# Performance work log

Hardware: AMD Instinct MI355X
Metric: run time of the kernel (lower is better)

## Reference

```python
import jax, jax.numpy as jnp
import numpy as np

B, R, T, F_IN, L, D, H, OUT, ES = 8, 128, 64, 32, 64, 64, 128, 32, 2048
DT = 0.1  # dt_step from init


def _glorot(key, shape):
    scale = 1.0 / np.sqrt(shape[0])
    return (jax.random.normal(key, shape, jnp.float32) * scale).astype(jnp.float32)


def setup_inputs() -> dict:
    key = jax.random.key(0)
    ks = jax.random.split(key, 20)
    return {
        "node_feats": jax.random.normal(ks[0], (B, R, T, F_IN), jnp.float32),
        "eps": jax.random.normal(ks[1], (B, R, L + D), jnp.float32),
        "space_w": jax.random.uniform(ks[2], (B, ES), jnp.float32),
        "src": jax.random.randint(ks[3], (ES,), 0, R, jnp.int32),
        "dst": jax.random.randint(ks[4], (ES,), 0, R, jnp.int32),
        "W_e1": _glorot(ks[5], (F_IN + 1, H)),
        "b_e1": jnp.zeros((H,), jnp.float32),
        "W_e2": _glorot(ks[6], (H, H)),
        "b_e2": jnp.zeros((H,), jnp.float32),
        "W_mu": _glorot(ks[7], (H, L + D)),
        "W_sig": _glorot(ks[8], (H, L + D)),
        "W_msg": _glorot(ks[9], (L, L)),
        "W_self": _glorot(ks[10], (L, L)),
        "W_dyn": _glorot(ks[11], (D, L)),
        "b_ode": jnp.zeros((L,), jnp.float32),
        "W_d1": _glorot(ks[12], (L + D + 1 + R, H)),
        "b_d1": jnp.zeros((H,), jnp.float32),
        "W_d2": _glorot(ks[13], (H, OUT)),
        "b_d2": jnp.zeros((OUT,), jnp.float32),
    }


def reference(node_feats, eps, space_w, src, dst,
              W_e1, b_e1, W_e2, b_e2, W_mu, W_sig,
              W_msg, W_self, W_dyn, b_ode,
              W_d1, b_d1, W_d2, b_d2):
    dt = jnp.asarray(DT, node_feats.dtype)
    tgrid = jnp.arange(T, dtype=node_feats.dtype) / T  # normalized time, like t/t.max()
    t_feat = jnp.broadcast_to(tgrid[None, None, :, None], (B, R, T, 1))

    # ---- Encoder: node features + time -> per-node mu/sigma (NP-style) ----
    x = jnp.concatenate([node_feats, t_feat], axis=-1)          # [B,R,T,F+1]
    h = jax.nn.silu(x @ W_e1 + b_e1)
    h = jax.nn.silu(h @ W_e2 + b_e2)
    hp = h.mean(axis=2)                                          # pool over time -> [B,R,H]
    mu = hp @ W_mu                                               # [B,R,L+D]
    sigma = 0.1 + 0.9 * jax.nn.sigmoid(hp @ W_sig)
    v = mu + sigma * eps                                         # reparameterized latent
    Lz, Dz = v[..., :L], v[..., L:]                              # integrated state / h_dyn

    # ---- MPGCN ODE func: weighted edge gather/scatter + self + h_dyn ----
    dyn = Dz @ W_dyn                                             # constant conditioning [B,R,L]

    def f(xs):                                                   # xs: [B,R,L]
        m = space_w[..., None] * xs[:, src, :]                   # per-edge message [B,E,L]
        agg = jnp.zeros((B, R, L), xs.dtype).at[:, dst].add(m)   # sum aggregation
        return jnp.tanh(agg @ W_msg + xs @ W_self + dyn + b_ode)

    # ---- RK4 fixed-step integrator, save state at every time point ----
    def step(xs, _):
        k1 = f(xs)
        k2 = f(xs + 0.5 * dt * k1)
        k3 = f(xs + 0.5 * dt * k2)
        k4 = f(xs + dt * k3)
        xn = xs + (dt / 6.0) * (k1 + 2.0 * k2 + 2.0 * k3 + k4)
        return xn, xn

    _, traj = jax.lax.scan(step, Lz, None, length=T)             # [T,B,R,L]
    traj = jnp.moveaxis(traj, 0, 2)                              # [B,R,T,L]

    # ---- Decoder: [L(t), h_dyn, time, region one-hot] -> y ----
    rid = jnp.broadcast_to(jnp.eye(R, dtype=traj.dtype)[None, :, None, :], (B, R, T, R))
    d_rep = jnp.broadcast_to(Dz[:, :, None, :], (B, R, T, D))
    dec_in = jnp.concatenate([traj, d_rep, t_feat, rid], axis=-1)  # [B,R,T,257]
    hd = jax.nn.silu(dec_in @ W_d1 + b_d1)
    y = hd @ W_d2 + b_d2                                         # [B,R,T,OUT]
    return y
```

## Files before the change

### kernel.cpp

```cpp
#include <hip/hip_runtime.h>

#define B_ 8
#define R_ 128
#define T_ 64
#define FIN_ 32
#define L_ 64
#define D_ 64
#define H_ 128
#define OUT_ 32
#define ES_ 2048

typedef _Float16 f16;
typedef __attribute__((ext_vector_type(2))) _Float16 f16x2;
typedef __attribute__((ext_vector_type(4))) _Float16 f16x4;
typedef __attribute__((ext_vector_type(8))) _Float16 f16x8;
typedef __attribute__((ext_vector_type(16))) float f32x16;

__device__ __forceinline__ float silu_f(float x) { return x / (1.f + __expf(-x)); }
__device__ __forceinline__ float tanh_f(float x) {
    float e = __expf(2.f * x);
    return 1.f - 2.f / (e + 1.f);
}

__device__ __forceinline__ uint32_t swz256(uint32_t row, uint32_t s, uint32_t colByte) {
    uint32_t bo = row * 256u + s * 128u + colByte;
    return bo ^ ((row & 15u) << 4);
}
__device__ __forceinline__ uint32_t swzT(uint32_t c, uint32_t s, uint32_t rByte) {
    uint32_t bo = c * 512u + s * 256u + rByte;
    return bo ^ ((c & 31u) << 4);
}

#define XROW_OFF 0u
#define MT_OFF   32768u
#define WS_OFF   65536u
#define WM_OFF   81920u
#define ODE_LDS  98304u

__global__ __launch_bounds__(128) void prep_kernel(
    const int* __restrict__ src, const int* __restrict__ dst,
    const float* __restrict__ space_w,
    int* __restrict__ row_start, int* __restrict__ esrcp, float* __restrict__ wperm) {
    __shared__ int cnt[R_];
    __shared__ int rs[R_ + 1];
    __shared__ int permS[ES_];
    int r = threadIdx.x;
    int c = 0;
    for (int e = 0; e < ES_; ++e) c += (dst[e] == r) ? 1 : 0;
    cnt[r] = c;
    __syncthreads();
    if (r == 0) {
        int a = 0;
        for (int i = 0; i < R_; ++i) { rs[i] = a; a += cnt[i]; }
        rs[R_] = a;
    }
    __syncthreads();
    {
        int k = rs[r];
        for (int e = 0; e < ES_; ++e)
            if (dst[e] == r) permS[k++] = e;
    }
    __syncthreads();
    row_start[r] = rs[r];
    if (r == 0) row_start[R_] = rs[R_];
    for (int e = r; e < ES_; e += 128) esrcp[e] = src[permS[e]];
    for (int i = r; i < B_ * ES_; i += 128) {
        int b = i >> 11;
        int e = i & (ES_ - 1);
        wperm[i] = space_w[b * ES_ + permS[e]];
    }
}

__global__ __launch_bounds__(256) void encoder_kernel(
    const float* __restrict__ node_feats, const float* __restrict__ eps,
    const float* __restrict__ W_e1, const float* __restrict__ b_e1,
    const float* __restrict__ W_e2, const float* __restrict__ b_e2,
    const float* __restrict__ W_mu, const float* __restrict__ W_sig,
    const float* __restrict__ W_dyn,
    float* __restrict__ Lz, float* __restrict__ Dz, float* __restrict__ dynb) {
    int br = blockIdx.x;
    int tid = threadIdx.x;
    __shared__ __align__(16) float xS[T_ * 36];
    __shared__ __align__(16) float h1[T_ * H_];
    __shared__ float hps[2 * H_];
    __shared__ float hp[H_];
    __shared__ float muS[H_], sgS[H_], vS[H_];

    const float* nf = node_feats + (size_t)br * (T_ * FIN_);
    for (int i = tid; i < T_ * FIN_; i += 256) {
        int t = i >> 5, f = i & 31;
        xS[t * 36 + f] = nf[i];
    }
    if (tid < T_) xS[tid * 36 + 32] = (float)tid * (1.f / 64.f);

    int j = tid & 127;
    int th = tid >> 7;
    float we1r[33];
    #pragma unroll
    for (int k = 0; k < 33; ++k) we1r[k] = W_e1[k * H_ + j];
    __syncthreads();

    float be1 = b_e1[j];
    for (int tt = 0; tt < 32; ++tt) {
        int t = th * 32 + tt;
        float a = be1;
        const float4* xr = (const float4*)(&xS[t * 36]);
        #pragma unroll
        for (int w4 = 0; w4 < 8; ++w4) {
            float4 xv = xr[w4];
            a += xv.x * we1r[w4 * 4 + 0] + xv.y * we1r[w4 * 4 + 1] +
                 xv.z * we1r[w4 * 4 + 2] + xv.w * we1r[w4 * 4 + 3];
        }
        a += xS[t * 36 + 32] * we1r[32];
        h1[t * H_ + j] = silu_f(a);
    }
    __syncthreads();

    float acc[32];
    float be2 = b_e2[j];
    #pragma unroll
    for (int tt = 0; tt < 32; ++tt) acc[tt] = be2;
    for (int kc = 0; kc < 4; ++kc) {
        float wreg[32];
        #pragma unroll
        for (int i2 = 0; i2 < 32; ++i2) wreg[i2] = W_e2[(kc * 32 + i2) * H_ + j];
        #pragma unroll
        for (int tt = 0; tt < 32; ++tt) {
            int t = th * 32 + tt;
            const float4* hrow = (const float4*)(&h1[t * H_ + kc * 32]);
            float s = 0.f;
            #pragma unroll
            for (int w4 = 0; w4 < 8; ++w4) {
                float4 hv = hrow[w4];
                s += hv.x * wreg[w4 * 4 + 0] + hv.y * wreg[w4 * 4 + 1] +
                     hv.z * wreg[w4 * 4 + 2] + hv.w * wreg[w4 * 4 + 3];
            }
            acc[tt] += s;
        }
    }
    float msum = 0.f;
    #pragma unroll
    for (int tt = 0; tt < 32; ++tt) msum += silu_f(acc[tt]);
    hps[th * H_ + j] = msum;
    __syncthreads();
    if (tid < H_) hp[tid] = (hps[tid] + hps[H_ + tid]) * (1.f / 64.f);
    __syncthreads();

    {
        const float* Wm = (th == 0) ? W_mu : W_sig;
        float a = 0.f;
        #pragma unroll 4
        for (int k = 0; k < H_; ++k) a += hp[k] * Wm[k * H_ + j];
        if (th == 0) muS[j] = a; else sgS[j] = a;
    }
    __syncthreads();
    if (tid < H_) {
        float sig = 0.1f + 0.9f / (1.f + __expf(-sgS[tid]));
        float v = muS[tid] + sig * eps[(size_t)br * H_ + tid];
        vS[tid] = v;
        if (tid < L_) Lz[(size_t)br * L_ + tid] = v;
        else          Dz[(size_t)br * D_ + (tid - L_)] = v;
    }
    __syncthreads();
    if (tid < L_) {
        float a = 0.f;
        #pragma unroll 4
        for (int k = 0; k < D_; ++k) a += vS[L_ + k] * W_dyn[k * L_ + tid];
        dynb[(size_t)br * L_ + tid] = a;
    }
}

__global__ __launch_bounds__(512, 2) void ode_kernel(
    const float* __restrict__ Lz, const float* __restrict__ dynb,
    const float* __restrict__ W_msg, const float* __restrict__ W_self,
    const float* __restrict__ b_ode,
    const int* __restrict__ row_start, const int* __restrict__ esrcp,
    const float* __restrict__ wperm,
    float* __restrict__ traj) {
    const int b = blockIdx.x;
    const int tid = threadIdx.x;
    const int lane = tid & 63;
    const int w = tid >> 6;
    const int rb = w & 3;
    const int cb = w >> 2;
    const int l31 = lane & 31;
    const int h = lane >> 5;
    const int cc = cb * 32 + l31;

    extern __shared__ char sm[];
    float* Af = (float*)sm;

    for (int idx = tid; idx < 4096; idx += 512) {
        int j = idx & 63, k = idx >> 6;
        float vs = W_self[k * 64 + j];
        f16 sh = (f16)vs;
        *(f16*)(sm + WS_OFF + swz256(j, 0, k * 2)) = sh;
        *(f16*)(sm + WS_OFF + swz256(j, 1, k * 2)) = (f16)(vs - (float)sh);
        float vm = W_msg[k * 64 + j];
        f16 mh = (f16)vm;
        *(f16*)(sm + WM_OFF + swz256(j, 0, k * 2)) = mh;
        *(f16*)(sm + WM_OFF + swz256(j, 1, k * 2)) = (f16)(vm - (float)mh);
    }
    for (int i = tid; i < 128 * 128; i += 512) Af[i] = 0.f;
    __syncthreads();
    if (tid < 128) {
        int e0 = row_start[tid], e1 = row_start[tid + 1];
        for (int e = e0; e < e1; ++e)
            Af[tid * 128 + esrcp[e]] += wperm[b * ES_ + e];
    }
    __syncthreads();

    f16x8 aH[8], aL[8];
    {
        int row = rb * 32 + l31;
        #pragma unroll
        for (int m = 0; m < 8; ++m) {
            const float* p = Af + row * 128 + m * 16 + h * 8;
            f16x8 vh, vl;
            #pragma unroll
            for (int i = 0; i < 8; ++i) {
                float v = p[i];
                f16 hi = (f16)v;
                vh[i] = hi;
                vl[i] = (f16)(v - (float)hi);
            }
            aH[m] = vh;
            aL[m] = vl;
        }
    }

    float xb[16], ks[16], dnb[16];
    {
        float bo = b_ode[cc];
        #pragma unroll
        for (int i = 0; i < 16; ++i) {
            int r = rb * 32 + (i & 3) + 8 * (i >> 2) + 4 * h;
            size_t o = ((size_t)(b * R_ + r)) * L_ + cc;
            xb[i] = Lz[o];
            dnb[i] = dynb[o] + bo;
        }
    }
    __syncthreads();

    #pragma unroll
    for (int i = 0; i < 16; ++i) {
        int r = rb * 32 + (i & 3) + 8 * (i >> 2) + 4 * h;
        f16 hi = (f16)xb[i];
        *(f16*)(sm + XROW_OFF + swz256(r, 0, cc * 2)) = hi;
        *(f16*)(sm + XROW_OFF + swz256(r, 1, cc * 2)) = (f16)(xb[i] - (float)hi);
    }
    __syncthreads();

    const int rowx = rb * 32 + l31;

    for (int n = 0; n < T_; ++n) {
        #pragma unroll
        for (int i = 0; i < 16; ++i) ks[i] = 0.f;
        for (int s4 = 0; s4 < 4; ++s4) {
            const float wk = (s4 == 1 || s4 == 2) ? 2.f : 1.f;
            const float cn = (s4 < 2) ? 0.05f : 0.1f;

            f16x8 xh[4], xl[4];
            #pragma unroll
            for (int m = 0; m < 4; ++m) {
                uint32_t kB = (m * 16 + 8 * h) * 2;
                xh[m] = *(const f16x8*)(sm + XROW_OFF + swz256(rowx, 0, kB));
                xl[m] = *(const f16x8*)(sm + XROW_OFF + swz256(rowx, 1, kB));
            }
            f32x16 aS, aM = {};
            #pragma unroll
            for (int i = 0; i < 16; ++i) aS[i] = dnb[i];
            #pragma unroll
            for (int m = 0; m < 4; ++m) {
                uint32_t kB = (m * 16 + 8 * h) * 2;
                f16x8 wsH = *(const f16x8*)(sm + WS_OFF + swz256(cc, 0, kB));
                f16x8 wsL = *(const f16x8*)(sm + WS_OFF + swz256(cc, 1, kB));
                f16x8 wmH = *(const f16x8*)(sm + WM_OFF + swz256(cc, 0, kB));
                f16x8 wmL = *(const f16x8*)(sm + WM_OFF + swz256(cc, 1, kB));
                aS = __builtin_amdgcn_mfma_f32_32x32x16_f16(xh[m], wsH, aS, 0, 0, 0);
                aM = __builtin_amdgcn_mfma_f32_32x32x16_f16(xh[m], wmH, aM, 0, 0, 0);
                aS = __builtin_amdgcn_mfma_f32_32x32x16_f16(xl[m], wsH, aS, 0, 0, 0);
                aM = __builtin_amdgcn_mfma_f32_32x32x16_f16(xl[m], wmH, aM, 0, 0, 0);
                aS = __builtin_amdgcn_mfma_f32_32x32x16_f16(xh[m], wsL, aS, 0, 0, 0);
                aM = __builtin_amdgcn_mfma_f32_32x32x16_f16(xh[m], wmL, aM, 0, 0, 0);
            }
            #pragma unroll
            for (int q = 0; q < 4; ++q) {
                int rbase = rb * 32 + 8 * q + 4 * h;
                f16x4 vh, vl;
                #pragma unroll
                for (int u = 0; u < 4; ++u) {
                    float t = aM[4 * q + u];
                    f16 hi = (f16)t;
                    vh[u] = hi;
                    vl[u] = (f16)(t - (float)hi);
                }
                *(f16x4*)(sm + MT_OFF + swzT(cc, 0, rbase * 2)) = vh;
                *(f16x4*)(sm + MT_OFF + swzT(cc, 1, rbase * 2)) = vl;
            }
            __syncthreads();

            f32x16 e0 = {}, e1 = {}, e2 = {};
            #pragma unroll
            for (int m = 0; m < 8; ++m) {
                f16x8 mtH = *(const f16x8*)(sm + MT_OFF + swzT(cc, 0, (m * 16 + 8 * h) * 2));
                f16x8 mtL = *(const f16x8*)(sm + MT_OFF + swzT(cc, 1, (m * 16 + 8 * h) * 2));
                if (m < 3) {
                    e0 = __builtin_amdgcn_mfma_f32_32x32x16_f16(aH[m], mtH, e0, 0, 0, 0);
                    e0 = __builtin_amdgcn_mfma_f32_32x32x16_f16(aL[m], mtH, e0, 0, 0, 0);
                    e0 = __builtin_amdgcn_mfma_f32_32x32x16_f16(aH[m], mtL, e0, 0, 0, 0);
                } else if (m < 6) {
                    e1 = __builtin_amdgcn_mfma_f32_32x32x16_f16(aH[m], mtH, e1, 0, 0, 0);
                    e1 = __builtin_amdgcn_mfma_f32_32x32x16_f16(aL[m], mtH, e1, 0, 0, 0);
                    e1 = __builtin_amdgcn_mfma_f32_32x32x16_f16(aH[m], mtL, e1, 0, 0, 0);
                } else {
                    e2 = __builtin_amdgcn_mfma_f32_32x32x16_f16(aH[m], mtH, e2, 0, 0, 0);
                    e2 = __builtin_amdgcn_mfma_f32_32x32x16_f16(aL[m], mtH, e2, 0, 0, 0);
                    e2 = __builtin_amdgcn_mfma_f32_32x32x16_f16(aH[m], mtL, e2, 0, 0, 0);
                }
            }
            float xn_[16];
            #pragma unroll
            for (int i = 0; i < 16; ++i) {
                float kv = tanh_f(aS[i] + e0[i] + e1[i] + e2[i]);
                ks[i] += wk * kv;
                xn_[i] = (s4 < 3) ? (xb[i] + cn * kv) : (xb[i] + (0.1f / 6.f) * ks[i]);
            }
            if (s4 == 3) {
                #pragma unroll
                for (int i = 0; i < 16; ++i) xb[i] = xn_[i];
            }
            #pragma unroll
            for (int i = 0; i < 16; ++i) {
                int r = rb * 32 + (i & 3) + 8 * (i >> 2) + 4 * h;
                f16 hi = (f16)xn_[i];
                *(f16*)(sm + XROW_OFF + swz256(r, 0, cc * 2)) = hi;
                *(f16*)(sm + XROW_OFF + swz256(r, 1, cc * 2)) = (f16)(xn_[i] - (float)hi);
            }
            if (s4 == 3) {
                #pragma unroll
                for (int i = 0; i < 16; ++i) {
                    int r = rb * 32 + (i & 3) + 8 * (i >> 2) + 4 * h;
                    traj[(((size_t)b * T_ + n) * R_ + r) * L_ + cc] = xb[i];
                }
            }
            __syncthreads();
        }
    }
}

__global__ __launch_bounds__(256) void decoder_kernel(
    const float* __restrict__ traj, const float* __restrict__ Dz,
    const float* __restrict__ W_d1, const float* __restrict__ b_d1,
    const float* __restrict__ W_d2, const float* __restrict__ b_d2,
    float* __restrict__ y) {
    int br = blockIdx.x;
    int b = br >> 7;
    int r = br & 127;
    int tid = threadIdx.x;
    __shared__ __align__(16) float trajS[32 * L_];
    __shared__ __align__(16) float hS[32 * H_];
    __shared__ float dzS[D_];
    __shared__ float baseS[H_];

    int j = tid & 127;
    int th = tid >> 7;
    if (tid < D_) dzS[tid] = Dz[(size_t)br * D_ + tid];
    __syncthreads();

    float wcol[64];
    #pragma unroll
    for (int k = 0; k < 64; ++k) wcol[k] = W_d1[k * H_ + j];
    float wt = W_d1[128 * H_ + j];
    if (th == 0) {
        float a = b_d1[j] + W_d1[(129 + r) * H_ + j];
        #pragma unroll 4
        for (int k = 0; k < D_; ++k) a += dzS[k] * W_d1[(64 + k) * H_ + j];
        baseS[j] = a;
    }
    __syncthreads();
    float bb = baseS[j];

    for (int half = 0; half < 2; ++half) {
        for (int i = tid; i < 32 * L_; i += 256) {
            int tt = i >> 6, l = i & 63;
            trajS[i] = traj[(((size_t)b * T_ + half * 32 + tt) * R_ + r) * L_ + l];
        }
        __syncthreads();
        #pragma unroll
        for (int tt = 0; tt < 16; ++tt) {
            int tl = th * 16 + tt;
            int t = half * 32 + tl;
            float a = bb + (float)t * (1.f / 64.f) * wt;
            const float4* tr4 = (const float4*)(&trajS[tl * L_]);
            #pragma unroll
            for (int kb = 0; kb < 16; ++kb) {
                float4 tv = tr4[kb];
                a += tv.x * wcol[kb * 4 + 0] + tv.y * wcol[kb * 4 + 1] +
                     tv.z * wcol[kb * 4 + 2] + tv.w * wcol[kb * 4 + 3];
            }
            hS[tl * H_ + j] = silu_f(a);
        }
        __syncthreads();
        {
            int o = tid & 31, q = tid >> 5;
            float acc2[4];
            float bd2 = b_d2[o];
            #pragma unroll
            for (int u = 0; u < 4; ++u) acc2[u] = bd2;
            for (int jc = 0; jc < 4; ++jc) {
                float wreg[32];
                #pragma unroll
                for (int i2 = 0; i2 < 32; ++i2) wreg[i2] = W_d2[(jc * 32 + i2) * OUT_ + o];
                #pragma unroll
                for (int u = 0; u < 4; ++u) {
                    int tl = q * 4 + u;
                    const float4* h4 = (const float4*)(&hS[tl * H_ + jc * 32]);
                    float s2 = 0.f;
                    #pragma unroll
                    for (int w4 = 0; w4 < 8; ++w4) {
                        float4 hv = h4[w4];
                        s2 += hv.x * wreg[w4 * 4 + 0] + hv.y * wreg[w4 * 4 + 1] +
                              hv.z * wreg[w4 * 4 + 2] + hv.w * wreg[w4 * 4 + 3];
                    }
                    acc2[u] += s2;
                }
            }
            #pragma unroll
            for (int u = 0; u < 4; ++u) {
                int t = half * 32 + q * 4 + u;
                y[((size_t)br * T_ + t) * OUT_ + o] = acc2[u];
            }
        }
        __syncthreads();
    }
}

extern "C" void kernel_launch(void* const* d_in, const int* in_sizes, int n_in,
                              void* d_out, int out_size, void* d_ws, size_t ws_size,
                              hipStream_t stream) {
    const float* node_feats = (const float*)d_in[0];
    const float* eps_       = (const float*)d_in[1];
    const float* space_w    = (const float*)d_in[2];
    const int*   src        = (const int*)d_in[3];
    const int*   dst        = (const int*)d_in[4];
    const float* W_e1 = (const float*)d_in[5];
    const float* b_e1 = (const float*)d_in[6];
    const float* W_e2 = (const float*)d_in[7];
    const float* b_e2 = (const float*)d_in[8];
    const float* W_mu = (const float*)d_in[9];
    const float* W_sig = (const float*)d_in[10];
    const float* W_msg = (const float*)d_in[11];
    const float* W_self = (const float*)d_in[12];
    const float* W_dyn = (const float*)d_in[13];
    const float* b_ode = (const float*)d_in[14];
    const float* W_d1 = (const float*)d_in[15];
    const float* b_d1 = (const float*)d_in[16];
    const float* W_d2 = (const float*)d_in[17];
    const float* b_d2 = (const float*)d_in[18];
    float* out = (float*)d_out;

    float* f_ws = (float*)d_ws;
    float* Lz    = f_ws;
    float* Dz    = Lz + B_ * R_ * L_;
    float* dynb  = Dz + B_ * R_ * D_;
    float* traj  = dynb + B_ * R_ * L_;
    float* wperm = traj + (size_t)B_ * T_ * R_ * L_;
    int* row_start = (int*)(wperm + B_ * ES_);
    int* esrcp     = row_start + 132;

    prep_kernel<<<1, 128, 0, stream>>>(src, dst, space_w, row_start, esrcp, wperm);
    encoder_kernel<<<B_ * R_, 256, 0, stream>>>(node_feats, eps_, W_e1, b_e1, W_e2, b_e2,
                                                W_mu, W_sig, W_dyn, Lz, Dz, dynb);
    ode_kernel<<<B_, 512, ODE_LDS, stream>>>(Lz, dynb, W_msg, W_self, b_ode,
                                             row_start, esrcp, wperm, traj);
    decoder_kernel<<<B_ * R_, 256, 0, stream>>>(traj, Dz, W_d1, b_d1, W_d2, b_d2, out);
}
```

Measured before the change: 1.639 ms.

## Fold edge-sort prep into ODE kernel, keep high weight halves in registers, prefetch MT

Result: slower. 1.981 ms (+20.9%).

```diff
diff --git a/kernel.cpp b/kernel.cpp
--- a/kernel.cpp
+++ b/kernel.cpp
@@ -33,43 +33,9 @@
 
 #define XROW_OFF 0u
 #define MT_OFF   32768u
-#define WS_OFF   65536u
-#define WM_OFF   81920u
-#define ODE_LDS  98304u
-
-__global__ __launch_bounds__(128) void prep_kernel(
-    const int* __restrict__ src, const int* __restrict__ dst,
-    const float* __restrict__ space_w,
-    int* __restrict__ row_start, int* __restrict__ esrcp, float* __restrict__ wperm) {
-    __shared__ int cnt[R_];
-    __shared__ int rs[R_ + 1];
-    __shared__ int permS[ES_];
-    int r = threadIdx.x;
-    int c = 0;
-    for (int e = 0; e < ES_; ++e) c += (dst[e] == r) ? 1 : 0;
-    cnt[r] = c;
-    __syncthreads();
-    if (r == 0) {
-        int a = 0;
-        for (int i = 0; i < R_; ++i) { rs[i] = a; a += cnt[i]; }
-        rs[R_] = a;
-    }
-    __syncthreads();
-    {
-        int k = rs[r];
-        for (int e = 0; e < ES_; ++e)
-            if (dst[e] == r) permS[k++] = e;
-    }
-    __syncthreads();
-    row_start[r] = rs[r];
-    if (r == 0) row_start[R_] = rs[R_];
-    for (int e = r; e < ES_; e += 128) esrcp[e] = src[permS[e]];
-    for (int i = r; i < B_ * ES_; i += 128) {
-        int b = i >> 11;
-        int e = i & (ES_ - 1);
-        wperm[i] = space_w[b * ES_ + permS[e]];
-    }
-}
+#define WLO_OFF  65536u
+#define PRM_OFF  81920u
+#define ODE_LDS  91648u
 
 __global__ __launch_bounds__(256) void encoder_kernel(
     const float* __restrict__ node_feats, const float* __restrict__ eps,
@@ -174,8 +140,8 @@
     const float* __restrict__ Lz, const float* __restrict__ dynb,
     const float* __restrict__ W_msg, const float* __restrict__ W_self,
     const float* __restrict__ b_ode,
-    const int* __restrict__ row_start, const int* __restrict__ esrcp,
-    const float* __restrict__ wperm,
+    const int* __restrict__ src, const int* __restrict__ dst,
+    const float* __restrict__ space_w,
     float* __restrict__ traj) {
     const int b = blockIdx.x;
     const int tid = threadIdx.x;
@@ -189,24 +155,55 @@
 
     extern __shared__ char sm[];
     float* Af = (float*)sm;
+    int* permS = (int*)(sm + PRM_OFF);
+    int* cntS  = permS + ES_;
+    int* rsS   = cntS + R_;
 
     for (int idx = tid; idx < 4096; idx += 512) {
         int j = idx & 63, k = idx >> 6;
         float vs = W_self[k * 64 + j];
-        f16 sh = (f16)vs;
-        *(f16*)(sm + WS_OFF + swz256(j, 0, k * 2)) = sh;
-        *(f16*)(sm + WS_OFF + swz256(j, 1, k * 2)) = (f16)(vs - (float)sh);
+        *(f16*)(sm + WLO_OFF + swz256(j, 0, k * 2)) = (f16)(vs - (float)((f16)vs));
         float vm = W_msg[k * 64 + j];
-        f16 mh = (f16)vm;
-        *(f16*)(sm + WM_OFF + swz256(j, 0, k * 2)) = mh;
-        *(f16*)(sm + WM_OFF + swz256(j, 1, k * 2)) = (f16)(vm - (float)mh);
+        *(f16*)(sm + WLO_OFF + swz256(j, 1, k * 2)) = (f16)(vm - (float)((f16)vm));
+    }
+    f16x8 wsH[4], wmH[4];
+    #pragma unroll
+    for (int m = 0; m < 4; ++m) {
+        f16x8 sh_, mh_;
+        #pragma unroll
+        for (int i = 0; i < 8; ++i) {
+            int k = m * 16 + 8 * h + i;
+            sh_[i] = (f16)W_self[k * 64 + cc];
+            mh_[i] = (f16)W_msg[k * 64 + cc];
+        }
+        wsH[m] = sh_; wmH[m] = mh_;
+    }
+
+    if (tid < R_) {
+        int c = 0;
+        for (int e = 0; e < ES_; ++e) c += (dst[e] == tid) ? 1 : 0;
+        cntS[tid] = c;
+    }
+    __syncthreads();
+    if (tid == 0) {
+        int a = 0;
+        for (int i = 0; i < R_; ++i) { rsS[i] = a; a += cntS[i]; }
+        rsS[R_] = a;
+    }
+    __syncthreads();
+    if (tid < R_) {
+        int k = rsS[tid];
+        for (int e = 0; e < ES_; ++e)
+            if (dst[e] == tid) permS[k++] = e;
     }
     for (int i = tid; i < 128 * 128; i += 512) Af[i] = 0.f;
     __syncthreads();
-    if (tid < 128) {
-        int e0 = row_start[tid], e1 = row_start[tid + 1];
-        for (int e = e0; e < e1; ++e)
-            Af[tid * 128 + esrcp[e]] += wperm[b * ES_ + e];
+    if (tid < R_) {
+        int e0 = rsS[tid], e1 = rsS[tid + 1];
+        for (int e = e0; e < e1; ++e) {
+            int pe = permS[e];
+            Af[tid * 128 + src[pe]] += space_w[b * ES_ + pe];
+        }
     }
     __syncthreads();
 
@@ -273,16 +270,14 @@
             #pragma unroll
             for (int m = 0; m < 4; ++m) {
                 uint32_t kB = (m * 16 + 8 * h) * 2;
-                f16x8 wsH = *(const f16x8*)(sm + WS_OFF + swz256(cc, 0, kB));
-                f16x8 wsL = *(const f16x8*)(sm + WS_OFF + swz256(cc, 1, kB));
-                f16x8 wmH = *(const f16x8*)(sm + WM_OFF + swz256(cc, 0, kB));
-                f16x8 wmL = *(const f16x8*)(sm + WM_OFF + swz256(cc, 1, kB));
-                aS = __builtin_amdgcn_mfma_f32_32x32x16_f16(xh[m], wsH, aS, 0, 0, 0);
-                aM = __builtin_amdgcn_mfma_f32_32x32x16_f16(xh[m], wmH, aM, 0, 0, 0);
-                aS = __builtin_amdgcn_mfma_f32_32x32x16_f16(xl[m], wsH, aS, 0, 0, 0);
-                aM = __builtin_amdgcn_mfma_f32_32x32x16_f16(xl[m], wmH, aM, 0, 0, 0);
-                aS = __builtin_amdgcn_mfma_f32_32x32x16_f16(xh[m], wsL, aS, 0, 0, 0);
-                aM = __builtin_amdgcn_mfma_f32_32x32x16_f16(xh[m], wmL, aM, 0, 0, 0);
+                f16x8 wsl = *(const f16x8*)(sm + WLO_OFF + swz256(cc, 0, kB));
+                f16x8 wml = *(const f16x8*)(sm + WLO_OFF + swz256(cc, 1, kB));
+                aS = __builtin_amdgcn_mfma_f32_32x32x16_f16(xh[m], wsH[m], aS, 0, 0, 0);
+                aM = __builtin_amdgcn_mfma_f32_32x32x16_f16(xh[m], wmH[m], aM, 0, 0, 0);
+                aS = __builtin_amdgcn_mfma_f32_32x32x16_f16(xl[m], wsH[m], aS, 0, 0, 0);
+                aM = __builtin_amdgcn_mfma_f32_32x32x16_f16(xl[m], wmH[m], aM, 0, 0, 0);
+                aS = __builtin_amdgcn_mfma_f32_32x32x16_f16(xh[m], wsl, aS, 0, 0, 0);
+                aM = __builtin_amdgcn_mfma_f32_32x32x16_f16(xh[m], wml, aM, 0, 0, 0);
             }
             #pragma unroll
             for (int q = 0; q < 4; ++q) {
@@ -301,23 +296,29 @@
             __syncthreads();
 
             f32x16 e0 = {}, e1 = {}, e2 = {};
+            f16x8 cH = *(const f16x8*)(sm + MT_OFF + swzT(cc, 0, (8 * h) * 2));
+            f16x8 cL = *(const f16x8*)(sm + MT_OFF + swzT(cc, 1, (8 * h) * 2));
+            f16x8 nH, nL;
             #pragma unroll
             for (int m = 0; m < 8; ++m) {
-                f16x8 mtH = *(const f16x8*)(sm + MT_OFF + swzT(cc, 0, (m * 16 + 8 * h) * 2));
-                f16x8 mtL = *(const f16x8*)(sm + MT_OFF + swzT(cc, 1, (m * 16 + 8 * h) * 2));
-                if (m < 3) {
-                    e0 = __builtin_amdgcn_mfma_f32_32x32x16_f16(aH[m], mtH, e0, 0, 0, 0);
-                    e0 = __builtin_amdgcn_mfma_f32_32x32x16_f16(aL[m], mtH, e0, 0, 0, 0);
-                    e0 = __builtin_amdgcn_mfma_f32_32x32x16_f16(aH[m], mtL, e0, 0, 0, 0);
-                } else if (m < 6) {
-                    e1 = __builtin_amdgcn_mfma_f32_32x32x16_f16(aH[m], mtH, e1, 0, 0, 0);
-                    e1 = __builtin_amdgcn_mfma_f32_32x32x16_f16(aL[m], mtH, e1, 0, 0, 0);
-                    e1 = __builtin_amdgcn_mfma_f32_32x32x16_f16(aH[m], mtL, e1, 0, 0, 0);
+                if (m < 7) {
+                    nH = *(const f16x8*)(sm + MT_OFF + swzT(cc, 0, ((m + 1) * 16 + 8 * h) * 2));
+                    nL = *(const f16x8*)(sm + MT_OFF + swzT(cc, 1, ((m + 1) * 16 + 8 * h) * 2));
+                }
+                if (m % 3 == 0) {
+                    e0 = __builtin_amdgcn_mfma_f32_32x32x16_f16(aH[m], cH, e0, 0, 0, 0);
+                    e0 = __builtin_amdgcn_mfma_f32_32x32x16_f16(aL[m], cH, e0, 0, 0, 0);
+                    e0 = __builtin_amdgcn_mfma_f32_32x32x16_f16(aH[m], cL, e0, 0, 0, 0);
+                } else if (m % 3 == 1) {
+                    e1 = __builtin_amdgcn_mfma_f32_32x32x16_f16(aH[m], cH, e1, 0, 0, 0);
+                    e1 = __builtin_amdgcn_mfma_f32_32x32x16_f16(aL[m], cH, e1, 0, 0, 0);
+                    e1 = __builtin_amdgcn_mfma_f32_32x32x16_f16(aH[m], cL, e1, 0, 0, 0);
                 } else {
-                    e2 = __builtin_amdgcn_mfma_f32_32x32x16_f16(aH[m], mtH, e2, 0, 0, 0);
-                    e2 = __builtin_amdgcn_mfma_f32_32x32x16_f16(aL[m], mtH, e2, 0, 0, 0);
-                    e2 = __builtin_amdgcn_mfma_f32_32x32x16_f16(aH[m], mtL, e2, 0, 0, 0);
+                    e2 = __builtin_amdgcn_mfma_f32_32x32x16_f16(aH[m], cH, e2, 0, 0, 0);
+                    e2 = __builtin_amdgcn_mfma_f32_32x32x16_f16(aL[m], cH, e2, 0, 0, 0);
+                    e2 = __builtin_amdgcn_mfma_f32_32x32x16_f16(aH[m], cL, e2, 0, 0, 0);
                 }
+                cH = nH; cL = nL;
             }
             float xn_[16];
             #pragma unroll
@@ -465,14 +466,10 @@
     float* Dz    = Lz + B_ * R_ * L_;
     float* dynb  = Dz + B_ * R_ * D_;
     float* traj  = dynb + B_ * R_ * L_;
-    float* wperm = traj + (size_t)B_ * T_ * R_ * L_;
-    int* row_start = (int*)(wperm + B_ * ES_);
-    int* esrcp     = row_start + 132;
-
-    prep_kernel<<<1, 128, 0, stream>>>(src, dst, space_w, row_start, esrcp, wperm);
+
     encoder_kernel<<<B_ * R_, 256, 0, stream>>>(node_feats, eps_, W_e1, b_e1, W_e2, b_e2,
                                                 W_mu, W_sig, W_dyn, Lz, Dz, dynb);
     ode_kernel<<<B_, 512, ODE_LDS, stream>>>(Lz, dynb, W_msg, W_self, b_ode,
-                                             row_start, esrcp, wperm, traj);
+                                             src, dst, space_w, traj);
     decoder_kernel<<<B_ * R_, 256, 0, stream>>>(traj, Dz, W_d1, b_d1, W_d2, b_d2, out);
 }
```
